# Optimization experiments

Hardware: AMD Instinct MI355X
Metric: run time of the kernel (lower is better)

## Reference

```python
import jax, jax.numpy as jnp
import numpy as np

B, K, N = 8192, 4096, 4096
GROUP = 128
G = K // GROUP
NLEVELS = 16


def setup_inputs() -> dict:
    key = jax.random.key(0)
    k1, k2, k3, k4, k5 = jax.random.split(key, 5)
    x = jax.random.normal(k1, (B, K), dtype=jnp.float32)
    indices = jax.random.randint(k2, (N, K), 0, NLEVELS, dtype=jnp.int32)
    codebook = jax.random.normal(k3, (NLEVELS,), dtype=jnp.float32)
    weight_norms = jax.random.uniform(k4, (N, G), dtype=jnp.float32)
    # per-group orthogonal rotation matrices (QR of Gaussian, as in rotation='qr')
    A = jax.random.normal(k5, (G, GROUP, GROUP), dtype=jnp.float32)
    Q, _ = jnp.linalg.qr(A)  # (G, GROUP, GROUP)
    return {"x": x, "indices": indices, "codebook": codebook,
            "weight_norms": weight_norms, "rotations": Q}


def reference(x, indices, codebook, weight_norms, rotations):
    """TurboQuantLinear forward (single pass, no bias, no residual).

    For each group g:
      x_rot_g = x[:, gs:ge] @ Pi_g.T
      out    += (x_rot_g @ codebook[idx_g].T) * (norms[:, g] / sqrt(group_size))
    Vectorized over groups.
    """
    b, k = x.shape
    g, gs, _ = rotations.shape
    n = indices.shape[0]
    scale = jnp.sqrt(jnp.asarray(gs, dtype=x.dtype))
    xg = x.reshape(b, g, gs)                                   # (B, G, gs)
    x_rot = jnp.einsum('bgk,gjk->bgj', xg, rotations)          # x_g @ Pi_g.T
    W = codebook[indices].reshape(n, g, gs)                    # dequant (N, G, gs)
    out = jnp.einsum('bgj,ngj,ng->bn', x_rot, W, weight_norms) / scale
    return out
```

## Files before the change

### kernel.cpp

```cpp
#include <hip/hip_runtime.h>
#include <hip/hip_bf16.h>

#define B_DIM 8192
#define K_DIM 4096
#define N_DIM 4096
#define GROUP 128
#define NG    (K_DIM / GROUP)
#define INV_SQRT_GROUP 0.08838834764831845f

using bf16x8 = __attribute__((ext_vector_type(8))) short;
using f32x4  = __attribute__((ext_vector_type(4))) float;

__device__ inline unsigned short f2bf(float f) {
    union { float f; unsigned u; } v; v.f = f;
    unsigned r = v.u + 0x7fffu + ((v.u >> 16) & 1u);
    return (unsigned short)(r >> 16);
}

#define GLOAD_LDS16(gp, lp)                                                   \
    __builtin_amdgcn_global_load_lds(                                         \
        (__attribute__((address_space(1))) void*)(gp),                        \
        (__attribute__((address_space(3))) void*)(lp), 16, 0, 0)

#define BAR()                                                                 \
    {                                                                         \
        asm volatile("" ::: "memory");                                        \
        __builtin_amdgcn_s_barrier();                                         \
        asm volatile("" ::: "memory");                                        \
    }
#define LGKM0()  asm volatile("s_waitcnt lgkmcnt(0)" ::: "memory")
#define VMCNT(n) asm volatile("s_waitcnt vmcnt(" #n ")" ::: "memory")
#define PRIO(p)  __builtin_amdgcn_s_setprio(p)

__global__ __launch_bounds__(256) void cast_x_kernel(
    const float* __restrict__ x, unsigned short* __restrict__ xb, size_t n8)
{
    size_t i = (size_t)blockIdx.x * blockDim.x + threadIdx.x;
    if (i >= n8) return;
    const float4* xp = (const float4*)x;
    float4 a = xp[2 * i];
    float4 b = xp[2 * i + 1];
    union { unsigned short s[8]; uint4 v; } pk;
    pk.s[0] = f2bf(a.x); pk.s[1] = f2bf(a.y); pk.s[2] = f2bf(a.z); pk.s[3] = f2bf(a.w);
    pk.s[4] = f2bf(b.x); pk.s[5] = f2bf(b.y); pk.s[6] = f2bf(b.z); pk.s[7] = f2bf(b.w);
    ((uint4*)xb)[i] = pk.v;
}

__global__ __launch_bounds__(256) void cast_rot_kernel(
    const float* __restrict__ rot, unsigned short* __restrict__ Rt)
{
    const int g = blockIdx.x;
    const float* Rg = rot + (size_t)g * GROUP * GROUP;
    unsigned short* Rtg = Rt + (size_t)g * GROUP * GROUP;
    for (int e = threadIdx.x; e < 128 * 32; e += 256) {
        int j = e >> 5, kc = (e & 31) * 4;
        float4 v = *(const float4*)(Rg + (size_t)j * 128 + kc);
        Rtg[(size_t)(kc + 0) * 128 + j] = f2bf(v.x);
        Rtg[(size_t)(kc + 1) * 128 + j] = f2bf(v.y);
        Rtg[(size_t)(kc + 2) * 128 + j] = f2bf(v.z);
        Rtg[(size_t)(kc + 3) * 128 + j] = f2bf(v.w);
    }
}

__global__ __launch_bounds__(256) void prep_v_kernel(
    const int*   __restrict__ indices,
    const float* __restrict__ codebook,
    const float* __restrict__ norms,
    const unsigned short* __restrict__ Rt,
    unsigned short* __restrict__ Vout)
{
    const int g  = blockIdx.y;
    const int n0 = blockIdx.x * 128;
    const int tid = threadIdx.x;

    __shared__ __attribute__((aligned(16))) unsigned short w_lds[128][136];
    __shared__ float s_lds[128];
    __shared__ float cb_lds[16];

    if (tid < 16)  cb_lds[tid] = codebook[tid];
    if (tid < 128) s_lds[tid] = norms[(size_t)(n0 + tid) * NG + g] * INV_SQRT_GROUP;
    __syncthreads();

    for (int e = tid; e < 128 * 16; e += 256) {
        const int nl = e >> 4, jc = e & 15;
        const float s = s_lds[nl];
        const int4* ip = (const int4*)(indices + (size_t)(n0 + nl) * K_DIM + g * GROUP + jc * 8);
        int4 i0 = ip[0];
        int4 i1 = ip[1];
        union { unsigned short h[8]; uint4 v; } pk;
        pk.h[0] = f2bf(cb_lds[i0.x] * s); pk.h[1] = f2bf(cb_lds[i0.y] * s);
        pk.h[2] = f2bf(cb_lds[i0.z] * s); pk.h[3] = f2bf(cb_lds[i0.w] * s);
        pk.h[4] = f2bf(cb_lds[i1.x] * s); pk.h[5] = f2bf(cb_lds[i1.y] * s);
        pk.h[6] = f2bf(cb_lds[i1.z] * s); pk.h[7] = f2bf(cb_lds[i1.w] * s);
        *(uint4*)&w_lds[nl][jc * 8] = pk.v;
    }
    __syncthreads();

    const int lane = tid & 63;
    const int wv   = tid >> 6;
    const int l15  = lane & 15;
    const int quad = lane >> 4;
    const int wn = (wv >> 1) * 64;
    const int wk = (wv & 1) * 64;

    const unsigned short* Rtg = Rt + (size_t)g * GROUP * GROUP;

    f32x4 acc[4][4] = {};

    for (int js = 0; js < 4; ++js) {
        const int jo = js * 32 + quad * 8;
        bf16x8 aF[4], bF[4];
        for (int mi = 0; mi < 4; ++mi)
            aF[mi] = *(const bf16x8*)&w_lds[wn + mi * 16 + l15][jo];
        for (int ni = 0; ni < 4; ++ni) {
            const int k = wk + ni * 16 + l15;
            bF[ni] = *(const bf16x8*)(Rtg + (size_t)k * 128 + jo);
        }
        for (int mi = 0; mi < 4; ++mi)
            for (int ni = 0; ni < 4; ++ni)
                acc[mi][ni] = __builtin_amdgcn_mfma_f32_16x16x32_bf16(
                    aF[mi], bF[ni], acc[mi][ni], 0, 0, 0);
    }

    __syncthreads();

    for (int mi = 0; mi < 4; ++mi) {
        const int nl = wn + mi * 16 + quad * 4;
        for (int ni = 0; ni < 4; ++ni) {
            const int kl = wk + ni * 16 + l15;
            for (int r = 0; r < 4; ++r)
                w_lds[nl + r][kl] = f2bf(acc[mi][ni][r]);
        }
    }
    __syncthreads();

    {
        const int rlo = tid >> 4;
        const int col = (tid & 15) * 8;
        for (int pass = 0; pass < 8; ++pass) {
            const int row = pass * 16 + rlo;
            uint4 v = *(const uint4*)&w_lds[row][col];
            *(uint4*)(Vout + (size_t)(n0 + row) * K_DIM + g * GROUP + col) = v;
        }
    }
}

template <int GRP, int NLO>
__device__ __forceinline__ void mfma_quad(f32x4 (&acc)[8][4],
                                          const bf16x8 (&aF)[4][2],
                                          const bf16x8 (&bF)[4][2])
{
#pragma unroll
    for (int mi = 0; mi < 4; ++mi)
#pragma unroll
        for (int nn = 0; nn < 2; ++nn)
#pragma unroll
            for (int kh = 0; kh < 2; ++kh)
                acc[GRP * 4 + mi][NLO + nn] = __builtin_amdgcn_mfma_f32_16x16x32_bf16(
                    aF[mi][kh], bF[NLO + nn][kh], acc[GRP * 4 + mi][NLO + nn], 0, 0, 0);
}

__global__ __launch_bounds__(512) void gemm256_kernel(
    const unsigned short* __restrict__ A,
    const unsigned short* __restrict__ Bm,
    float* __restrict__ C)
{
    const int tid = threadIdx.x;

    const int flat = blockIdx.y * gridDim.x + blockIdx.x;
    const int swz  = (flat & 7) * 64 + (flat >> 3);
    const int n0 = (swz & 15) * 256;
    const int m0 = (swz >> 4) * 256;

    __shared__ __attribute__((aligned(16))) unsigned short a_lds[2 * 256 * 64];
    __shared__ __attribute__((aligned(16))) unsigned short b_lds[2 * 256 * 64];

    const int lane = tid & 63;
    const int wv   = tid >> 6;
    const int l15  = lane & 15;
    const int quad = lane >> 4;
    const int wm   = wv >> 2;
    const int wn   = wv & 3;

    int rr[4], ko[4], lb[4];
#pragma unroll
    for (int p = 0; p < 4; ++p) {
        int c = tid + 512 * p;
        rr[p] = c >> 3;
        ko[p] = ((c & 7) ^ ((c >> 3) & 7)) * 8;
        lb[p] = (tid & ~63) + 512 * p;
    }

    const int koh0 = ((0 * 4 + quad) ^ (l15 & 7)) * 8;
    const int koh1 = ((1 * 4 + quad) ^ (l15 & 7)) * 8;
    const int aBase = (wm * 128 + l15) * 64;
    const int bBase = (wn * 64 + l15) * 64;

    f32x4 acc[8][4] = {};
    bf16x8 aF[4][2], bF[4][2];

#define STAGE_A(bb, kt, p)                                                    \
    GLOAD_LDS16(A + (size_t)(m0 + rr[p]) * K_DIM + (size_t)(kt) * 64 + ko[p], \
                a_lds + (bb) * 16384 + lb[p] * 8)
#define STAGE_B(bb, kt, p)                                                    \
    GLOAD_LDS16(Bm + (size_t)(n0 + rr[p]) * K_DIM + (size_t)(kt) * 64 + ko[p],\
                b_lds + (bb) * 16384 + lb[p] * 8)

#pragma unroll
    for (int p = 0; p < 4; ++p) STAGE_A(0, 0, p);
#pragma unroll
    for (int p = 0; p < 4; ++p) STAGE_B(0, 0, p);
#pragma unroll
    for (int p = 0; p < 4; ++p) STAGE_A(1, 1, p);
#pragma unroll
    for (int p = 0; p < 4; ++p) STAGE_B(1, 1, p);
    VMCNT(8);
    BAR();

    for (int t = 0; t < 64; ++t) {
        const int b = t & 1;
        const int boff = b * 16384;

#pragma unroll
        for (int mi = 0; mi < 4; ++mi) {
            aF[mi][0] = *(const bf16x8*)&a_lds[boff + aBase + mi * 1024 + koh0];
            aF[mi][1] = *(const bf16x8*)&a_lds[boff + aBase + mi * 1024 + koh1];
        }
#pragma unroll
        for (int nn = 0; nn < 2; ++nn) {
            bF[nn][0] = *(const bf16x8*)&b_lds[boff + bBase + nn * 1024 + koh0];
            bF[nn][1] = *(const bf16x8*)&b_lds[boff + bBase + nn * 1024 + koh1];
        }
        BAR(); LGKM0();
        PRIO(1); mfma_quad<0, 0>(acc, aF, bF); PRIO(0);
        BAR();

#pragma unroll
        for (int nn = 2; nn < 4; ++nn) {
            bF[nn][0] = *(const bf16x8*)&b_lds[boff + bBase + nn * 1024 + koh0];
            bF[nn][1] = *(const bf16x8*)&b_lds[boff + bBase + nn * 1024 + koh1];
        }
        BAR(); LGKM0();
        PRIO(1); mfma_quad<0, 2>(acc, aF, bF); PRIO(0);
        BAR();

#pragma unroll
        for (int mi = 0; mi < 4; ++mi) {
            aF[mi][0] = *(const bf16x8*)&a_lds[boff + aBase + 4096 + mi * 1024 + koh0];
            aF[mi][1] = *(const bf16x8*)&a_lds[boff + aBase + 4096 + mi * 1024 + koh1];
        }
        if (t + 2 < 64) { STAGE_B(b, t + 2, 0); STAGE_B(b, t + 2, 1); }
        BAR(); LGKM0();
        PRIO(1); mfma_quad<1, 0>(acc, aF, bF); PRIO(0);
        BAR();

        if (t + 2 < 64) {
            STAGE_B(b, t + 2, 2); STAGE_B(b, t + 2, 3);
#pragma unroll
            for (int p = 0; p < 4; ++p) STAGE_A(b, t + 2, p);
        }
        BAR();
        PRIO(1); mfma_quad<1, 2>(acc, aF, bF); PRIO(0);
        if (t < 62)       { VMCNT(8); }
        else if (t == 62) { VMCNT(0); }
        BAR();
    }

#pragma unroll
    for (int mi = 0; mi < 8; ++mi) {
        int m = m0 + wm * 128 + mi * 16 + quad * 4;
#pragma unroll
        for (int ni = 0; ni < 4; ++ni) {
            int n = n0 + wn * 64 + ni * 16 + l15;
            float* dst = C + (size_t)m * N_DIM + n;
#pragma unroll
            for (int r = 0; r < 4; ++r)
                dst[(size_t)r * N_DIM] = acc[mi][ni][r];
        }
    }
#undef STAGE_A
#undef STAGE_B
}

extern "C" void kernel_launch(void* const* d_in, const int* in_sizes, int n_in,
                              void* d_out, int out_size, void* d_ws, size_t ws_size,
                              hipStream_t stream)
{
    const float* x        = (const float*)d_in[0];
    const int*   indices  = (const int*)d_in[1];
    const float* codebook = (const float*)d_in[2];
    const float* norms    = (const float*)d_in[3];
    const float* rot      = (const float*)d_in[4];
    float* out            = (float*)d_out;

    unsigned short* Rt = (unsigned short*)d_ws;
    unsigned short* Xb = Rt + (size_t)NG * GROUP * GROUP;
    unsigned short* V  = Xb + (size_t)B_DIM * K_DIM;

    {
        size_t n8 = (size_t)B_DIM * K_DIM / 8;
        cast_x_kernel<<<dim3((unsigned)(n8 / 256)), dim3(256), 0, stream>>>(x, Xb, n8);
        cast_rot_kernel<<<dim3(NG), dim3(256), 0, stream>>>(rot, Rt);
    }
    {
        dim3 grid(N_DIM / 128, NG);
        prep_v_kernel<<<grid, dim3(256), 0, stream>>>(indices, codebook, norms, Rt, V);
    }
    {
        dim3 grid(N_DIM / 256, B_DIM / 256);
        gemm256_kernel<<<grid, dim3(512), 0, stream>>>(Xb, V, out);
    }
}
```

Before: 583.3 us.

## Stage B tiles one step ahead, drop tile swizzle, coalesce epilogue via LDS

Three changes. Block-to-tile mapping now uses plain blockIdx instead of the XCD/L2-oriented swizzle. B-tile loads for step t+1 move into the first two phases of step t, writing the other buffer, while A stays two steps ahead; the vmcnt waits change to match. The epilogue passes accumulators through LDS with a padded row stride so each row is written with float4 stores, replacing scattered 4-byte stores. This aims to smooth global-load timing and cut write transactions, but removing the swizzle may hurt L2 locality, and the new prefetch/wait scheme risks races.

```diff
diff --git a/kernel.cpp b/kernel.cpp
--- a/kernel.cpp
+++ b/kernel.cpp
@@ -166,11 +166,8 @@
     float* __restrict__ C)
 {
     const int tid = threadIdx.x;
-
-    const int flat = blockIdx.y * gridDim.x + blockIdx.x;
-    const int swz  = (flat & 7) * 64 + (flat >> 3);
-    const int n0 = (swz & 15) * 256;
-    const int m0 = (swz >> 4) * 256;
+    const int n0 = blockIdx.x * 256;
+    const int m0 = blockIdx.y * 256;
 
     __shared__ __attribute__((aligned(16))) unsigned short a_lds[2 * 256 * 64];
     __shared__ __attribute__((aligned(16))) unsigned short b_lds[2 * 256 * 64];
@@ -212,9 +209,7 @@
     for (int p = 0; p < 4; ++p) STAGE_B(0, 0, p);
 #pragma unroll
     for (int p = 0; p < 4; ++p) STAGE_A(1, 1, p);
-#pragma unroll
-    for (int p = 0; p < 4; ++p) STAGE_B(1, 1, p);
-    VMCNT(8);
+    VMCNT(4);
     BAR();
 
     for (int t = 0; t < 64; ++t) {
@@ -231,6 +226,7 @@
             bF[nn][0] = *(const bf16x8*)&b_lds[boff + bBase + nn * 1024 + koh0];
             bF[nn][1] = *(const bf16x8*)&b_lds[boff + bBase + nn * 1024 + koh1];
         }
+        if (t + 1 < 64) { STAGE_B(b ^ 1, t + 1, 0); STAGE_B(b ^ 1, t + 1, 1); }
         BAR(); LGKM0();
         PRIO(1); mfma_quad<0, 0>(acc, aF, bF); PRIO(0);
         BAR();
@@ -240,6 +236,7 @@
             bF[nn][0] = *(const bf16x8*)&b_lds[boff + bBase + nn * 1024 + koh0];
             bF[nn][1] = *(const bf16x8*)&b_lds[boff + bBase + nn * 1024 + koh1];
         }
+        if (t + 1 < 64) { STAGE_B(b ^ 1, t + 1, 2); STAGE_B(b ^ 1, t + 1, 3); }
         BAR(); LGKM0();
         PRIO(1); mfma_quad<0, 2>(acc, aF, bF); PRIO(0);
         BAR();
@@ -249,33 +246,46 @@
             aF[mi][0] = *(const bf16x8*)&a_lds[boff + aBase + 4096 + mi * 1024 + koh0];
             aF[mi][1] = *(const bf16x8*)&a_lds[boff + aBase + 4096 + mi * 1024 + koh1];
         }
-        if (t + 2 < 64) { STAGE_B(b, t + 2, 0); STAGE_B(b, t + 2, 1); }
         BAR(); LGKM0();
         PRIO(1); mfma_quad<1, 0>(acc, aF, bF); PRIO(0);
         BAR();
 
         if (t + 2 < 64) {
-            STAGE_B(b, t + 2, 2); STAGE_B(b, t + 2, 3);
 #pragma unroll
             for (int p = 0; p < 4; ++p) STAGE_A(b, t + 2, p);
         }
         BAR();
         PRIO(1); mfma_quad<1, 2>(acc, aF, bF); PRIO(0);
-        if (t < 62)       { VMCNT(8); }
+        if (t < 62)       { VMCNT(4); }
         else if (t == 62) { VMCNT(0); }
         BAR();
     }
 
-#pragma unroll
-    for (int mi = 0; mi < 8; ++mi) {
-        int m = m0 + wm * 128 + mi * 16 + quad * 4;
-#pragma unroll
-        for (int ni = 0; ni < 4; ++ni) {
-            int n = n0 + wn * 64 + ni * 16 + l15;
-            float* dst = C + (size_t)m * N_DIM + n;
-#pragma unroll
-            for (int r = 0; r < 4; ++r)
-                dst[(size_t)r * N_DIM] = acc[mi][ni][r];
+    {
+        float* ct = (float*)a_lds;
+        const int trow = tid >> 4;
+        const int tc16 = tid & 15;
+#pragma unroll
+        for (int p = 0; p < 8; ++p) {
+            BAR();
+#pragma unroll
+            for (int ni = 0; ni < 4; ++ni) {
+                const int col = wn * 64 + ni * 16 + l15;
+#pragma unroll
+                for (int r = 0; r < 4; ++r) {
+                    const int jrow = wm * 16 + quad * 4 + r;
+                    ct[jrow * 260 + col] = acc[p][ni][r];
+                }
+            }
+            BAR();
+            const int m = m0 + (trow >> 4) * 128 + p * 16 + (trow & 15);
+            float* dst = C + (size_t)m * N_DIM + n0;
+            const float* src = ct + trow * 260;
+#pragma unroll
+            for (int s = 0; s < 4; ++s) {
+                const int cc = (tc16 + 16 * s) * 4;
+                *(float4*)&dst[cc] = *(const float4*)&src[cc];
+            }
         }
     }
 #undef STAGE_A
```

After: 534.9 us. 8.3% less time.
